# Optimization experiments

Hardware: AMD Instinct MI355X
Metric: run time of the kernel (lower is better)

## Reference

```python
import jax, jax.numpy as jnp
import numpy as np

N = 8192      # collocation points
H = 128       # hidden width of the stream-function MLP


def setup_inputs() -> dict:
    key = jax.random.key(0)
    ks = jax.random.split(key, 9)
    s = lambda fan_in: 1.0 / np.sqrt(fan_in)
    return {
        "x":  jax.random.normal(ks[0], (N, 3), dtype=jnp.float32),
        "W1": jax.random.normal(ks[1], (3, H), dtype=jnp.float32) * s(3),
        "b1": jnp.zeros((H,), dtype=jnp.float32),
        "W2": jax.random.normal(ks[2], (H, H), dtype=jnp.float32) * s(H),
        "b2": jnp.zeros((H,), dtype=jnp.float32),
        "W3": jax.random.normal(ks[3], (H, H), dtype=jnp.float32) * s(H),
        "b3": jnp.zeros((H,), dtype=jnp.float32),
        "W4": jax.random.normal(ks[4], (H, 1), dtype=jnp.float32) * s(H),
        "b4": jnp.zeros((1,), dtype=jnp.float32),
        "nu": jnp.float32(1.0),
    }


def reference(x, W1, b1, W2, b2, W3, b3, W4, b4, nu):
    # psi: scalar stream function of a single sample xi = (x, y, t)
    def psi(xi):
        h = jnp.tanh(xi @ W1 + b1)
        h = jnp.tanh(h @ W2 + b2)
        h = jnp.tanh(h @ W3 + b3)
        return (h @ W4 + b4)[0]

    # vorticity w = dv/dx - du/dy = -(psi_xx + psi_yy)
    def w_fn(xi):
        Hpsi = jax.hessian(psi)(xi)          # [3,3]
        return -(Hpsi[0, 0] + Hpsi[1, 1])

    def per_sample(xi):
        g = jax.grad(psi)(xi)                # dpsi: [3]
        u = g[1]
        v = -g[0]
        dw = jax.grad(w_fn)(xi)              # [dwdx, dwdy, dwdt]
        Hw = jax.hessian(w_fn)(xi)           # 4th-order derivs of psi
        lapw = Hw[0, 0] + Hw[1, 1]
        nse = dw[2] + dw[0] * u + dw[1] * v - nu * lapw
        return jnp.stack([u, v]), nse

    f, NSE = jax.vmap(per_sample)(x)         # f: [N,2], NSE: [N]
    return f, NSE
```

## Files before the change

### kernel.cpp

```cpp
#include <hip/hip_runtime.h>

#define NSAMP 8192
#define HD 128
#define NC 18
#define SB 8
#define NCOLS 144
#define KSTR 136

typedef __attribute__((ext_vector_type(8))) short bf16x8;
typedef __attribute__((ext_vector_type(4))) float f32x4;
typedef float f2 __attribute__((ext_vector_type(2)));


__device__ __forceinline__ unsigned pack_bf16_rne(float x, float y) {
    unsigned ux = __float_as_uint(x), uy = __float_as_uint(y);
    ux += 0x7fffu + ((ux >> 16) & 1u);
    uy += 0x7fffu + ((uy >> 16) & 1u);
    return (ux >> 16) | (uy & 0xffff0000u);
}
__device__ __forceinline__ float bf_lo(unsigned r) { return __uint_as_float(r << 16); }
__device__ __forceinline__ float bf_hi(unsigned r) { return __uint_as_float(r & 0xffff0000u); }

__device__ __forceinline__ void jmul(const float* __restrict__ p,
                                     const float* __restrict__ q,
                                     float* __restrict__ r) {
    r[0]  = p[0]*q[0];
    r[1]  = p[0]*q[1]  + p[1]*q[0];
    r[2]  = p[0]*q[2]  + p[2]*q[0];
    r[3]  = p[0]*q[3]  + p[3]*q[0];
    r[4]  = p[0]*q[4]  + p[4]*q[0]  + p[1]*q[1];
    r[5]  = p[0]*q[5]  + p[5]*q[0]  + p[1]*q[2]  + p[2]*q[1];
    r[6]  = p[0]*q[6]  + p[6]*q[0]  + p[2]*q[2];
    r[7]  = p[0]*q[7]  + p[7]*q[0]  + p[1]*q[3]  + p[3]*q[1];
    r[8]  = p[0]*q[8]  + p[8]*q[0]  + p[2]*q[3]  + p[3]*q[2];
    r[9]  = p[0]*q[9]  + p[9]*q[0]  + p[1]*q[4]  + p[4]*q[1];
    r[10] = p[0]*q[10] + p[10]*q[0] + p[1]*q[5]  + p[5]*q[1] + p[2]*q[4] + p[4]*q[2];
    r[11] = p[0]*q[11] + p[11]*q[0] + p[1]*q[6]  + p[6]*q[1] + p[2]*q[5] + p[5]*q[2];
    r[12] = p[0]*q[12] + p[12]*q[0] + p[2]*q[6]  + p[6]*q[2];
    r[13] = p[0]*q[13] + p[13]*q[0] + p[1]*q[7]  + p[7]*q[1] + p[3]*q[4] + p[4]*q[3];
    r[14] = p[0]*q[14] + p[14]*q[0] + p[2]*q[8]  + p[8]*q[2] + p[3]*q[6] + p[6]*q[3];
    r[15] = p[0]*q[15] + p[15]*q[0] + p[1]*q[9]  + p[9]*q[1] + p[4]*q[4];
    r[16] = p[0]*q[16] + p[16]*q[0] + p[1]*q[11] + p[11]*q[1] + p[2]*q[10] + p[10]*q[2]
          + p[4]*q[6]  + p[6]*q[4]  + p[5]*q[5];
    r[17] = p[0]*q[17] + p[17]*q[0] + p[2]*q[12] + p[12]*q[2] + p[6]*q[6];
}

__device__ __forceinline__ void tanh_jet(const float* __restrict__ f,
                                         float* __restrict__ out) {
    const float y  = tanhf(f[0]);
    const float s  = 1.0f - y*y;
    const float t2 = -y*s;
    const float t3 = s*(y*y - 0.3333333333333333f);
    const float t4 = y*s*(2.0f - 3.0f*y*y) * 0.3333333333333333f;
    float p[NC], A[NC], B[NC];
    p[0] = 0.0f;
#pragma unroll
    for (int i = 1; i < NC; ++i) p[i] = f[i];
    A[0] = t3;
#pragma unroll
    for (int i = 1; i < NC; ++i) A[i] = t4 * p[i];
    jmul(p, A, B);  B[0] += t2;
    jmul(p, B, A);  A[0] += s;
    jmul(p, A, out); out[0] += y;
}

__global__ __launch_bounds__(256)
void transpose_w(const float* __restrict__ W2, const float* __restrict__ W3,
                 unsigned* __restrict__ wsT) {
    const int id = blockIdx.x * 256 + threadIdx.x;
    if (id >= 2 * HD * (KSTR / 2)) return;
    const int L  = id / (HD * (KSTR / 2));
    const int r  = id % (HD * (KSTR / 2));
    const int j  = r / (KSTR / 2);
    const int kp = r % (KSTR / 2);
    const int k0 = 2 * kp, k1 = 2 * kp + 1;
    const float* W = L ? W3 : W2;
    const float f0 = (k0 < HD) ? W[k0 * HD + j] : 0.0f;
    const float f1 = (k1 < HD) ? W[k1 * HD + j] : 0.0f;
    wsT[L * (HD * (KSTR / 2)) + j * (KSTR / 2) + kp] = pack_bf16_rne(f0, f1);
}

__global__ __launch_bounds__(512, 4)
void hydro_main(const float* __restrict__ x,
                const float* __restrict__ W1, const float* __restrict__ b1,
                const float* __restrict__ b2, const float* __restrict__ b3,
                const float* __restrict__ W4, const float* __restrict__ nu_p,
                const unsigned short* __restrict__ wsT,
                float* __restrict__ out) {
    __shared__ __align__(16) unsigned short Hl[NCOLS * KSTR];
    __shared__ float psis[NCOLS];

    const int tid = threadIdx.x;
    const int wv  = tid >> 6;
    const int ln  = tid & 63;
    const int s0  = blockIdx.x * SB;

    {
        const int s  = tid >> 6;
        const int jp = tid & 63;
        const float xs = x[3 * (s0 + s) + 0];
        const float ys = x[3 * (s0 + s) + 1];
        const float ts = x[3 * (s0 + s) + 2];
        float ha[NC], hb[NC], f[NC];
#pragma unroll
        for (int c = 0; c < NC; ++c) f[c] = 0.0f;
        int j = 2 * jp;
        float wx = W1[j], wy = W1[HD + j], wt = W1[2 * HD + j];
        f[0] = fmaf(wx, xs, fmaf(wy, ys, fmaf(wt, ts, b1[j])));
        f[1] = wx; f[2] = wy; f[3] = wt;
        tanh_jet(f, ha);
        j = 2 * jp + 1;
        wx = W1[j]; wy = W1[HD + j]; wt = W1[2 * HD + j];
        f[0] = fmaf(wx, xs, fmaf(wy, ys, fmaf(wt, ts, b1[j])));
        f[1] = wx; f[2] = wy; f[3] = wt;
        tanh_jet(f, hb);
#pragma unroll
        for (int c = 0; c < NC; ++c)
            *(unsigned*)&Hl[(s * NC + c) * KSTR + 2 * jp] = pack_bf16_rne(ha[c], hb[c]);
    }
    __syncthreads();

#pragma unroll 1
    for (int L = 0; L < 2; ++L) {
        const unsigned short* WT = wsT + L * HD * KSTR;
        const int mrow = 16 * wv + (ln & 15);
        const int koff = (ln >> 4) * 8;
        bf16x8 Af[4];
#pragma unroll
        for (int ks = 0; ks < 4; ++ks)
            Af[ks] = *(const bf16x8*)&WT[mrow * KSTR + ks * 32 + koff];
        f32x4 acc[9];
#pragma unroll
        for (int nt = 0; nt < 9; ++nt) acc[nt] = (f32x4)0.0f;
#pragma unroll
        for (int ks = 0; ks < 4; ++ks) {
#pragma unroll
            for (int nt = 0; nt < 9; ++nt) {
                const bf16x8 Bf = *(const bf16x8*)&Hl[(nt * 16 + (ln & 15)) * KSTR + ks * 32 + koff];
                acc[nt] = __builtin_amdgcn_mfma_f32_16x16x32_bf16(Af[ks], Bf, acc[nt], 0, 0, 0);
            }
        }
        __syncthreads();
#pragma unroll
        for (int nt = 0; nt < 9; ++nt) {
            const int n = nt * 16 + (ln & 15);
            const int m = 16 * wv + (ln >> 4) * 4;
            uint2 w;
            w.x = pack_bf16_rne(acc[nt].x, acc[nt].y);
            w.y = pack_bf16_rne(acc[nt].z, acc[nt].w);
            *(uint2*)&Hl[n * KSTR + m] = w;
        }
        __syncthreads();
        {
            const float* bL = L ? b3 : b2;
            const int s  = tid >> 6;
            const int jp = tid & 63;
            float fa[NC], fb[NC], ha[NC], hb[NC];
#pragma unroll
            for (int c = 0; c < NC; ++c) {
                const unsigned q = *(const unsigned*)&Hl[(s * NC + c) * KSTR + 2 * jp];
                fa[c] = bf_lo(q);
                fb[c] = bf_hi(q);
            }
            fa[0] += bL[2 * jp];
            fb[0] += bL[2 * jp + 1];
            tanh_jet(fa, ha);
            tanh_jet(fb, hb);
#pragma unroll
            for (int c = 0; c < NC; ++c)
                *(unsigned*)&Hl[(s * NC + c) * KSTR + 2 * jp] = pack_bf16_rne(ha[c], hb[c]);
        }
        __syncthreads();
    }

    if (tid < NCOLS) {
        float acc = 0.0f;
#pragma unroll
        for (int kk = 0; kk < 16; ++kk) {
            const uint4 q = *(const uint4*)&Hl[tid * KSTR + kk * 8];
            const int k = kk * 8;
            acc = fmaf(bf_lo(q.x), W4[k + 0], acc);
            acc = fmaf(bf_hi(q.x), W4[k + 1], acc);
            acc = fmaf(bf_lo(q.y), W4[k + 2], acc);
            acc = fmaf(bf_hi(q.y), W4[k + 3], acc);
            acc = fmaf(bf_lo(q.z), W4[k + 4], acc);
            acc = fmaf(bf_hi(q.z), W4[k + 5], acc);
            acc = fmaf(bf_lo(q.w), W4[k + 6], acc);
            acc = fmaf(bf_hi(q.w), W4[k + 7], acc);
        }
        psis[tid] = acc;
    }
    __syncthreads();

    if (tid < SB) {
        const float* p = &psis[tid * NC];
        const float nu = nu_p[0];
        const float u  = p[2];
        const float v  = -p[1];
        const float wx = -(6.0f * p[9]  + 2.0f * p[11]);
        const float wy = -(2.0f * p[10] + 6.0f * p[12]);
        const float wt = -(2.0f * p[13] + 2.0f * p[14]);
        const float lapw = -(24.0f * p[15] + 8.0f * p[16] + 24.0f * p[17]);
        const float nse  = wt + wx * u + wy * v - nu * lapw;
        const int gi = s0 + tid;
        out[2 * gi]         = u;
        out[2 * gi + 1]     = v;
        out[2 * NSAMP + gi] = nse;
    }
}

extern "C" void kernel_launch(void* const* d_in, const int* in_sizes, int n_in,
                              void* d_out, int out_size, void* d_ws, size_t ws_size,
                              hipStream_t stream) {
    const float* x  = (const float*)d_in[0];
    const float* W1 = (const float*)d_in[1];
    const float* b1 = (const float*)d_in[2];
    const float* W2 = (const float*)d_in[3];
    const float* b2 = (const float*)d_in[4];
    const float* W3 = (const float*)d_in[5];
    const float* b3 = (const float*)d_in[6];
    const float* W4 = (const float*)d_in[7];
    const float* nu = (const float*)d_in[9];
    float* out = (float*)d_out;

    unsigned* wsT = (unsigned*)d_ws;
    {
        const int total = 2 * HD * (KSTR / 2);
        hipLaunchKernelGGL(transpose_w, dim3((total + 255) / 256), dim3(256), 0, stream,
                           W2, W3, wsT);
    }
    hipLaunchKernelGGL(hydro_main, dim3(NSAMP / SB), dim3(512), 0, stream,
                       x, W1, b1, b2, b3, W4, nu,
                       (const unsigned short*)d_ws, out);
}
```

Baseline: 106.7 us.

## Fuse weight transpose into main kernel and vectorize tanh jets as float2

Removes the separate transpose_w launch. Each block now reads W2/W3 directly from global memory with strided fp32 loads and converts them to bf16 MFMA A-fragments in registers. The Taylor-jet tanh propagation is rewritten to process two hidden units at once with float2 vectors, aiming at packed FP32 math. bf16 packing switches to the HIP intrinsic. This trades one kernel launch for redundant strided weight loads and conversions in all 1024 blocks.

```diff
diff --git a/kernel.cpp b/kernel.cpp
--- a/kernel.cpp
+++ b/kernel.cpp
@@ -1,4 +1,5 @@
 #include <hip/hip_runtime.h>
+#include <hip/hip_bf16.h>
 
 #define NSAMP 8192
 #define HD 128
@@ -12,18 +13,20 @@
 typedef float f2 __attribute__((ext_vector_type(2)));
 
 
-__device__ __forceinline__ unsigned pack_bf16_rne(float x, float y) {
-    unsigned ux = __float_as_uint(x), uy = __float_as_uint(y);
-    ux += 0x7fffu + ((ux >> 16) & 1u);
-    uy += 0x7fffu + ((uy >> 16) & 1u);
-    return (ux >> 16) | (uy & 0xffff0000u);
-}
-__device__ __forceinline__ float bf_lo(unsigned r) { return __uint_as_float(r << 16); }
-__device__ __forceinline__ float bf_hi(unsigned r) { return __uint_as_float(r & 0xffff0000u); }
-
-__device__ __forceinline__ void jmul(const float* __restrict__ p,
-                                     const float* __restrict__ q,
-                                     float* __restrict__ r) {
+__device__ __forceinline__ unsigned packf2(f2 v) {
+    __hip_bfloat162 h = __float22bfloat162_rn(float2{v.x, v.y});
+    return *(unsigned*)&h;
+}
+__device__ __forceinline__ f2 unpk(unsigned r) {
+    f2 v;
+    v.x = __uint_as_float(r << 16);
+    v.y = __uint_as_float(r & 0xffff0000u);
+    return v;
+}
+
+__device__ __forceinline__ void jmul2(const f2* __restrict__ p,
+                                      const f2* __restrict__ q,
+                                      f2* __restrict__ r) {
     r[0]  = p[0]*q[0];
     r[1]  = p[0]*q[1]  + p[1]*q[0];
     r[2]  = p[0]*q[2]  + p[2]*q[0];
@@ -45,47 +48,32 @@
     r[17] = p[0]*q[17] + p[17]*q[0] + p[2]*q[12] + p[12]*q[2] + p[6]*q[6];
 }
 
-__device__ __forceinline__ void tanh_jet(const float* __restrict__ f,
-                                         float* __restrict__ out) {
-    const float y  = tanhf(f[0]);
-    const float s  = 1.0f - y*y;
-    const float t2 = -y*s;
-    const float t3 = s*(y*y - 0.3333333333333333f);
-    const float t4 = y*s*(2.0f - 3.0f*y*y) * 0.3333333333333333f;
-    float p[NC], A[NC], B[NC];
-    p[0] = 0.0f;
+__device__ __forceinline__ void tanh_jet2(const f2* __restrict__ f,
+                                          f2* __restrict__ out) {
+    f2 y;  y.x = tanhf(f[0].x);  y.y = tanhf(f[0].y);
+    const f2 one = {1.0f, 1.0f};
+    const f2 s  = one - y*y;
+    const f2 t2 = -y*s;
+    const f2 t3 = s*(y*y - 0.3333333333333333f);
+    const f2 t4 = y*s*(one + one - 3.0f*y*y) * 0.3333333333333333f;
+    f2 p[NC], A[NC], B[NC];
+    p[0] = (f2)0.0f;
 #pragma unroll
     for (int i = 1; i < NC; ++i) p[i] = f[i];
     A[0] = t3;
 #pragma unroll
     for (int i = 1; i < NC; ++i) A[i] = t4 * p[i];
-    jmul(p, A, B);  B[0] += t2;
-    jmul(p, B, A);  A[0] += s;
-    jmul(p, A, out); out[0] += y;
-}
-
-__global__ __launch_bounds__(256)
-void transpose_w(const float* __restrict__ W2, const float* __restrict__ W3,
-                 unsigned* __restrict__ wsT) {
-    const int id = blockIdx.x * 256 + threadIdx.x;
-    if (id >= 2 * HD * (KSTR / 2)) return;
-    const int L  = id / (HD * (KSTR / 2));
-    const int r  = id % (HD * (KSTR / 2));
-    const int j  = r / (KSTR / 2);
-    const int kp = r % (KSTR / 2);
-    const int k0 = 2 * kp, k1 = 2 * kp + 1;
-    const float* W = L ? W3 : W2;
-    const float f0 = (k0 < HD) ? W[k0 * HD + j] : 0.0f;
-    const float f1 = (k1 < HD) ? W[k1 * HD + j] : 0.0f;
-    wsT[L * (HD * (KSTR / 2)) + j * (KSTR / 2) + kp] = pack_bf16_rne(f0, f1);
+    jmul2(p, A, B);  B[0] += t2;
+    jmul2(p, B, A);  A[0] += s;
+    jmul2(p, A, out); out[0] += y;
 }
 
 __global__ __launch_bounds__(512, 4)
 void hydro_main(const float* __restrict__ x,
                 const float* __restrict__ W1, const float* __restrict__ b1,
-                const float* __restrict__ b2, const float* __restrict__ b3,
+                const float* __restrict__ W2, const float* __restrict__ b2,
+                const float* __restrict__ W3, const float* __restrict__ b3,
                 const float* __restrict__ W4, const float* __restrict__ nu_p,
-                const unsigned short* __restrict__ wsT,
                 float* __restrict__ out) {
     __shared__ __align__(16) unsigned short Hl[NCOLS * KSTR];
     __shared__ float psis[NCOLS];
@@ -94,41 +82,46 @@
     const int wv  = tid >> 6;
     const int ln  = tid & 63;
     const int s0  = blockIdx.x * SB;
+    const int s   = tid >> 6;
+    const int jp  = tid & 63;
 
     {
-        const int s  = tid >> 6;
-        const int jp = tid & 63;
         const float xs = x[3 * (s0 + s) + 0];
         const float ys = x[3 * (s0 + s) + 1];
         const float ts = x[3 * (s0 + s) + 2];
-        float ha[NC], hb[NC], f[NC];
-#pragma unroll
-        for (int c = 0; c < NC; ++c) f[c] = 0.0f;
-        int j = 2 * jp;
-        float wx = W1[j], wy = W1[HD + j], wt = W1[2 * HD + j];
-        f[0] = fmaf(wx, xs, fmaf(wy, ys, fmaf(wt, ts, b1[j])));
+        const int j0 = 2 * jp;
+        const f2 wx = *(const f2*)&W1[j0];
+        const f2 wy = *(const f2*)&W1[HD + j0];
+        const f2 wt = *(const f2*)&W1[2 * HD + j0];
+        const f2 bb = *(const f2*)&b1[j0];
+        f2 f[NC], h[NC];
+#pragma unroll
+        for (int c = 0; c < NC; ++c) f[c] = (f2)0.0f;
+        f[0] = wx * xs + wy * ys + wt * ts + bb;
         f[1] = wx; f[2] = wy; f[3] = wt;
-        tanh_jet(f, ha);
-        j = 2 * jp + 1;
-        wx = W1[j]; wy = W1[HD + j]; wt = W1[2 * HD + j];
-        f[0] = fmaf(wx, xs, fmaf(wy, ys, fmaf(wt, ts, b1[j])));
-        f[1] = wx; f[2] = wy; f[3] = wt;
-        tanh_jet(f, hb);
+        tanh_jet2(f, h);
 #pragma unroll
         for (int c = 0; c < NC; ++c)
-            *(unsigned*)&Hl[(s * NC + c) * KSTR + 2 * jp] = pack_bf16_rne(ha[c], hb[c]);
+            *(unsigned*)&Hl[(s * NC + c) * KSTR + j0] = packf2(h[c]);
     }
     __syncthreads();
 
 #pragma unroll 1
     for (int L = 0; L < 2; ++L) {
-        const unsigned short* WT = wsT + L * HD * KSTR;
-        const int mrow = 16 * wv + (ln & 15);
+        const float* __restrict__ W = L ? W3 : W2;
+        const int jj   = 16 * wv + (ln & 15);
         const int koff = (ln >> 4) * 8;
         bf16x8 Af[4];
 #pragma unroll
-        for (int ks = 0; ks < 4; ++ks)
-            Af[ks] = *(const bf16x8*)&WT[mrow * KSTR + ks * 32 + koff];
+        for (int ks = 0; ks < 4; ++ks) {
+            union { uint4 u; bf16x8 v; } cv;
+            const int kb = ks * 32 + koff;
+            cv.u.x = packf2(f2{W[(kb + 0) * HD + jj], W[(kb + 1) * HD + jj]});
+            cv.u.y = packf2(f2{W[(kb + 2) * HD + jj], W[(kb + 3) * HD + jj]});
+            cv.u.z = packf2(f2{W[(kb + 4) * HD + jj], W[(kb + 5) * HD + jj]});
+            cv.u.w = packf2(f2{W[(kb + 6) * HD + jj], W[(kb + 7) * HD + jj]});
+            Af[ks] = cv.v;
+        }
         f32x4 acc[9];
 #pragma unroll
         for (int nt = 0; nt < 9; ++nt) acc[nt] = (f32x4)0.0f;
@@ -146,29 +139,23 @@
             const int n = nt * 16 + (ln & 15);
             const int m = 16 * wv + (ln >> 4) * 4;
             uint2 w;
-            w.x = pack_bf16_rne(acc[nt].x, acc[nt].y);
-            w.y = pack_bf16_rne(acc[nt].z, acc[nt].w);
+            w.x = packf2(f2{acc[nt].x, acc[nt].y});
+            w.y = packf2(f2{acc[nt].z, acc[nt].w});
             *(uint2*)&Hl[n * KSTR + m] = w;
         }
         __syncthreads();
         {
             const float* bL = L ? b3 : b2;
-            const int s  = tid >> 6;
-            const int jp = tid & 63;
-            float fa[NC], fb[NC], ha[NC], hb[NC];
-#pragma unroll
-            for (int c = 0; c < NC; ++c) {
-                const unsigned q = *(const unsigned*)&Hl[(s * NC + c) * KSTR + 2 * jp];
-                fa[c] = bf_lo(q);
-                fb[c] = bf_hi(q);
-            }
-            fa[0] += bL[2 * jp];
-            fb[0] += bL[2 * jp + 1];
-            tanh_jet(fa, ha);
-            tanh_jet(fb, hb);
+            const int j0 = 2 * jp;
+            f2 fa[NC], ha[NC];
 #pragma unroll
             for (int c = 0; c < NC; ++c)
-                *(unsigned*)&Hl[(s * NC + c) * KSTR + 2 * jp] = pack_bf16_rne(ha[c], hb[c]);
+                fa[c] = unpk(*(const unsigned*)&Hl[(s * NC + c) * KSTR + j0]);
+            fa[0] += *(const f2*)&bL[j0];
+            tanh_jet2(fa, ha);
+#pragma unroll
+            for (int c = 0; c < NC; ++c)
+                *(unsigned*)&Hl[(s * NC + c) * KSTR + j0] = packf2(ha[c]);
         }
         __syncthreads();
     }
@@ -179,14 +166,15 @@
         for (int kk = 0; kk < 16; ++kk) {
             const uint4 q = *(const uint4*)&Hl[tid * KSTR + kk * 8];
             const int k = kk * 8;
-            acc = fmaf(bf_lo(q.x), W4[k + 0], acc);
-            acc = fmaf(bf_hi(q.x), W4[k + 1], acc);
-            acc = fmaf(bf_lo(q.y), W4[k + 2], acc);
-            acc = fmaf(bf_hi(q.y), W4[k + 3], acc);
-            acc = fmaf(bf_lo(q.z), W4[k + 4], acc);
-            acc = fmaf(bf_hi(q.z), W4[k + 5], acc);
-            acc = fmaf(bf_lo(q.w), W4[k + 6], acc);
-            acc = fmaf(bf_hi(q.w), W4[k + 7], acc);
+            const f2 e0 = unpk(q.x), e1 = unpk(q.y), e2 = unpk(q.z), e3 = unpk(q.w);
+            acc = fmaf(e0.x, W4[k + 0], acc);
+            acc = fmaf(e0.y, W4[k + 1], acc);
+            acc = fmaf(e1.x, W4[k + 2], acc);
+            acc = fmaf(e1.y, W4[k + 3], acc);
+            acc = fmaf(e2.x, W4[k + 4], acc);
+            acc = fmaf(e2.y, W4[k + 5], acc);
+            acc = fmaf(e3.x, W4[k + 6], acc);
+            acc = fmaf(e3.y, W4[k + 7], acc);
         }
         psis[tid] = acc;
     }
@@ -223,13 +211,6 @@
     const float* nu = (const float*)d_in[9];
     float* out = (float*)d_out;
 
-    unsigned* wsT = (unsigned*)d_ws;
-    {
-        const int total = 2 * HD * (KSTR / 2);
-        hipLaunchKernelGGL(transpose_w, dim3((total + 255) / 256), dim3(256), 0, stream,
-                           W2, W3, wsT);
-    }
     hipLaunchKernelGGL(hydro_main, dim3(NSAMP / SB), dim3(512), 0, stream,
-                       x, W1, b1, b2, b3, W4, nu,
-                       (const unsigned short*)d_ws, out);
-}
+                       x, W1, b1, W2, b2, W3, b3, W4, nu, out);
+}
```

After: 100.8 us. 5.6% less time.
